# Optimization experiments

Hardware: AMD Instinct MI355X
Metric: run time of the kernel (lower is better)

Reference implementation:

```python
import jax, jax.numpy as jnp
import numpy as np

B, S, H, NH = 2, 2048, 1024, 16
HD = H // NH


def setup_inputs() -> dict:
    key = jax.random.key(0)
    ks = jax.random.split(key, 14)
    lim = 1.0 / np.sqrt(H)  # torch Linear default init range
    def lin(ka, kb):
        W = jax.random.uniform(ka, (H, H), jnp.float32, -lim, lim)
        b = jax.random.uniform(kb, (H,), jnp.float32, -lim, lim)
        return W, b
    Wq, bq = lin(ks[0], ks[1])
    Wk, bk = lin(ks[2], ks[3])
    Wv, bv = lin(ks[4], ks[5])
    Wo, bo = lin(ks[6], ks[7])
    return {
        "query": jax.random.normal(ks[8], (B, S, H), jnp.float32),
        "key": jax.random.normal(ks[9], (B, S, H), jnp.float32),
        "value": jax.random.normal(ks[10], (B, S, H), jnp.float32),
        "attn_mask": jax.random.randint(ks[11], (B, S, S), 0, 2).astype(bool),
        "relative_time": jax.random.normal(ks[12], (B, 1, S, S), jnp.float32),
        "Wq": Wq, "bq": bq, "Wk": Wk, "bk": bk,
        "Wv": Wv, "bv": bv, "Wo": Wo, "bo": bo,
    }


def reference(query, key, value, attn_mask, relative_time,
              Wq, bq, Wk, bk, Wv, bv, Wo, bo):
    Bq, Sq, _ = query.shape
    Skv = key.shape[1]
    # projections (torch Linear: x @ W^T + b)
    Q = (query @ Wq.T + bq).reshape(Bq, Sq, NH, HD).transpose(0, 2, 1, 3)
    K = (key @ Wk.T + bk).reshape(Bq, Skv, NH, HD).transpose(0, 2, 1, 3)
    V = (value @ Wv.T + bv).reshape(Bq, Skv, NH, HD).transpose(0, 2, 1, 3)
    scale = HD ** (-0.5)
    # NOTE: bias added BEFORE scaling, matching the original (non-standard)
    scores = jnp.einsum("bhqd,bhkd->bhqk", Q, K)
    scores = (scores + relative_time) * scale
    scores = jnp.where(attn_mask[:, None, :, :], scores, -jnp.inf)
    attn = jax.nn.softmax(scores.astype(jnp.float32), axis=-1).astype(scores.dtype)
    attn = jnp.nan_to_num(attn, nan=0.0)
    # dropout is identity in eval mode (dropout_rate applied only when training)
    out = jnp.einsum("bhqk,bhkd->bhqd", attn, V)
    out = out.transpose(0, 2, 1, 3).reshape(Bq, Sq, H)
    return out @ Wo.T + bo
```

## Files before the change

### kernel.cpp

```cpp
#include <hip/hip_runtime.h>
#include <hip/hip_bf16.h>

constexpr int BATCH = 2, SEQ = 2048, HDIM = 1024, NHEADS = 16, HEADD = 64;
constexpr int MROWS = BATCH * SEQ;
constexpr float QSCALE = 0.18033688011112042f;

typedef short short8  __attribute__((ext_vector_type(8)));
typedef float f32x4   __attribute__((ext_vector_type(4)));
typedef float f32x16  __attribute__((ext_vector_type(16)));
typedef int   int4v   __attribute__((ext_vector_type(4)));
typedef unsigned short ushort4v __attribute__((ext_vector_type(4)));

static __device__ __forceinline__ short f2bf(float f) {
    __hip_bfloat16 h = __float2bfloat16(f);
    return *reinterpret_cast<short*>(&h);
}

static __device__ __forceinline__ int cvt_pk_bf16(float a, float b) {
    int r;
    asm("v_cvt_pk_bf16_f32 %0, %1, %2" : "=v"(r) : "v"(a), "v"(b));
    return r;
}

static __device__ __forceinline__ float bfbits2f(unsigned short u) {
    return __builtin_bit_cast(float, (unsigned int)u << 16);
}

static __device__ __forceinline__ void gload_lds16(const void* g, void* l) {
    __builtin_amdgcn_global_load_lds(
        (const __attribute__((address_space(1))) unsigned int*)g,
        (__attribute__((address_space(3))) unsigned int*)l, 16, 0, 0);
}

__global__ void cvt_qkv_kernel(const float* __restrict__ q, const float* __restrict__ k,
                               const float* __restrict__ v, short* __restrict__ xq,
                               short* __restrict__ xk, short* __restrict__ xv, int n4) {
    int i = blockIdx.x * blockDim.x + threadIdx.x;
    const int stride = gridDim.x * blockDim.x;
    for (; i < 3 * n4; i += stride) {
        const float* in; short* out; int j = i;
        if (j >= 2 * n4)      { in = v; out = xv; j -= 2 * n4; }
        else if (j >= n4)     { in = k; out = xk; j -= n4; }
        else                  { in = q; out = xq; }
        const float4 val = reinterpret_cast<const float4*>(in)[j];
        short4 o;
        o.x = f2bf(val.x); o.y = f2bf(val.y); o.z = f2bf(val.z); o.w = f2bf(val.w);
        reinterpret_cast<short4*>(out)[j] = o;
    }
}

__global__ void cvt_w4_kernel(const float* __restrict__ w0, const float* __restrict__ w1,
                              const float* __restrict__ w2, const float* __restrict__ w3,
                              short* __restrict__ o0, short* __restrict__ o1,
                              short* __restrict__ o2, short* __restrict__ o3, int n4) {
    int i = blockIdx.x * blockDim.x + threadIdx.x;
    const int stride = gridDim.x * blockDim.x;
    for (; i < 4 * n4; i += stride) {
        const float* in; short* out; int j = i;
        if (j >= 3 * n4)      { in = w3; out = o3; j -= 3 * n4; }
        else if (j >= 2 * n4) { in = w2; out = o2; j -= 2 * n4; }
        else if (j >= n4)     { in = w1; out = o1; j -= n4; }
        else                  { in = w0; out = o0; }
        const float4 val = reinterpret_cast<const float4*>(in)[j];
        short4 o;
        o.x = f2bf(val.x); o.y = f2bf(val.y); o.z = f2bf(val.z); o.w = f2bf(val.w);
        reinterpret_cast<short4*>(out)[j] = o;
    }
}

__global__ void detect_mask_kernel(const unsigned int* __restrict__ m, int* flag) {
    const int tid = threadIdx.x;
    int gt1 = 0, isf = 0;
    for (int i = 0; i < 4; ++i) {
        unsigned int wv = m[tid + 256 * i];
        if (wv > 1u) gt1 = 1;
        if (wv == 0x3F800000u) isf = 1;
    }
    __shared__ int s_gt1, s_isf;
    if (tid == 0) { s_gt1 = 0; s_isf = 0; }
    __syncthreads();
    if (gt1) atomicOr(&s_gt1, 1);
    if (isf) atomicOr(&s_isf, 1);
    __syncthreads();
    if (tid == 0) flag[0] = s_gt1 ? (s_isf ? 2 : 1) : 0;
}

__global__ void fuse_rel_kernel(const float* __restrict__ rel, const void* __restrict__ mask,
                                const int* __restrict__ flag, short* __restrict__ rT,
                                int nThr) {
    const int f = flag[0];
    int i = blockIdx.x * blockDim.x + threadIdx.x;
    const int stride = gridDim.x * blockDim.x;
    for (; i < nThr; i += stride) {
        const int q    = i & 2047;
        const int kv16 = (i >> 11) & 127;
        const int b    = i >> 18;
        const long base = ((long)(b * 2048 + q)) * 2048 + kv16 * 16;
        float4 rv[4];
        #pragma unroll
        for (int g = 0; g < 4; ++g)
            rv[g] = *reinterpret_cast<const float4*>(rel + base + 4 * g);
        bool mk[16];
        if (f == 1) {
            const unsigned int* mp = (const unsigned int*)((const unsigned char*)mask + base);
            #pragma unroll
            for (int wd = 0; wd < 4; ++wd) {
                const unsigned int mw = mp[wd];
                #pragma unroll
                for (int s = 0; s < 4; ++s) mk[wd * 4 + s] = ((mw >> (8 * s)) & 0xffu) != 0;
            }
        } else if (f == 0) {
            const int* mp = (const int*)mask + base;
            #pragma unroll
            for (int j = 0; j < 16; ++j) mk[j] = mp[j] != 0;
        } else {
            const float* mp = (const float*)mask + base;
            #pragma unroll
            for (int j = 0; j < 16; ++j) mk[j] = mp[j] != 0.0f;
        }
        const float* rp = reinterpret_cast<const float*>(&rv[0]);
        #pragma unroll
        for (int g = 0; g < 4; ++g) {
            short4 o;
            short* op = reinterpret_cast<short*>(&o);
            #pragma unroll
            for (int j = 0; j < 4; ++j) {
                const int idx = 4 * g + j;
                op[j] = f2bf(mk[idx] ? rp[idx] * QSCALE : -1e30f);
            }
            *reinterpret_cast<short4*>(rT + (((long)(b * 512 + kv16 * 4 + g)) * 2048 + q) * 4) = o;
        }
    }
}

template<typename EPI>
static __device__ __forceinline__
void gemm_core(const short* A, const short* Bw, int K, int m0, int n0, EPI epi) {
    __shared__ short As[128 * 64];
    __shared__ short Bs[128 * 64];
    const int tid  = threadIdx.x;
    const int lane = tid & 63;
    const int w    = tid >> 6;
    const int lo   = lane & 15, hi = lane >> 4;
    const int wm   = w >> 1, wn = w & 1;

    f32x4 acc[4][4] = {};

    const int arow = tid >> 3;
    const int acol = (tid & 7) * 8;
    const long aBase = (long)(m0 + arow) * K + acol;
    const long bBase = (long)(n0 + arow) * K + acol;

    for (int k0 = 0; k0 < K; k0 += 64) {
        for (int i = 0; i < 4; ++i) {
            gload_lds16(A  + aBase + (long)i * 32 * K + k0, (char*)As + i * 4096 + tid * 16);
            gload_lds16(Bw + bBase + (long)i * 32 * K + k0, (char*)Bs + i * 4096 + tid * 16);
        }
        __syncthreads();
        for (int ks = 0; ks < 2; ++ks) {
            short8 af[4], bf[4];
            const int koff = ks * 32 + hi * 8;
            for (int fm = 0; fm < 4; ++fm)
                af[fm] = *reinterpret_cast<const short8*>(&As[(wm * 64 + fm * 16 + lo) * 64 + koff]);
            for (int fn = 0; fn < 4; ++fn)
                bf[fn] = *reinterpret_cast<const short8*>(&Bs[(wn * 64 + fn * 16 + lo) * 64 + koff]);
            for (int fm = 0; fm < 4; ++fm)
                for (int fn = 0; fn < 4; ++fn)
                    acc[fm][fn] = __builtin_amdgcn_mfma_f32_16x16x32_bf16(
                        af[fm], bf[fn], acc[fm][fn], 0, 0, 0);
        }
        __syncthreads();
    }

    for (int fm = 0; fm < 4; ++fm)
        for (int fn = 0; fn < 4; ++fn) {
            const int n = n0 + wn * 64 + fn * 16 + lo;
            const int mB = m0 + wm * 64 + fm * 16 + hi * 4;
            for (int r = 0; r < 4; ++r) epi(mB + r, n, acc[fm][fn][r]);
        }
}

__global__ __launch_bounds__(256, 2)
void qkv_gemm(const short* xq, const short* xk, const short* xv,
              const short* wq, const short* wk, const short* wv,
              const float* bq, const float* bk, const float* bv,
              short* Qb, short* Kb, short* Vt) {
    const int which = blockIdx.x >> 8;
    const int bid   = blockIdx.x & 255;
    const int m0 = (bid >> 3) << 7;
    const int n0 = (bid & 7) << 7;
    const short* A    = which == 0 ? xq : which == 1 ? xk : xv;
    const short* W    = which == 0 ? wq : which == 1 ? wk : wv;
    const float* bias = which == 0 ? bq : which == 1 ? bk : bv;
    short* C          = which == 0 ? Qb : which == 1 ? Kb : Vt;
    const float scale = which == 0 ? QSCALE : 1.0f;
    gemm_core(A, W, HDIM, m0, n0, [&](int m, int n, float v) {
        v = (v + bias[n]) * scale;
        const int b = m >> 11, s = m & (SEQ - 1);
        const int h = n >> 6, d = n & 63;
        long idx;
        if (which != 2) idx = (((long)(b * NHEADS + h)) * SEQ + s) * HEADD + d;
        else            idx = (((long)(b * NHEADS + h)) * HEADD + d) * SEQ + s;
        C[idx] = f2bf(v);
    });
}

__global__ __launch_bounds__(256, 2)
void out_gemm(const short* A, const short* W, const float* bias, float* Cout) {
    const int bid = blockIdx.x;
    const int m0 = (bid >> 3) << 7;
    const int n0 = (bid & 7) << 7;
    gemm_core(A, W, HDIM, m0, n0, [&](int m, int n, float v) {
        Cout[(long)m * HDIM + n] = v + bias[n];
    });
}

__global__ __launch_bounds__(256, 2)
void attn_fwd(const short* __restrict__ Qb, const short* __restrict__ Kb,
              const short* __restrict__ Vtb, const short* __restrict__ rT,
              short* __restrict__ Ob) {
    __shared__ short Ks[2][64 * 64];
    __shared__ short Vs[2][64 * 64];
    const int tid  = threadIdx.x;
    const int lane = tid & 63;
    const int wq   = tid >> 6;
    const int l31  = lane & 31, hi2 = lane >> 5;
    const int wg = ((blockIdx.x & 7) << 6) + (blockIdx.x >> 3);
    const int qt = wg & 15, h = (wg >> 4) & 15, b = wg >> 8;
    const int bh = b * NHEADS + h;
    const int q0 = qt * 128 + wq * 32 + l31;

    short8 qf[4];
    {
        const short* qp = Qb + ((long)bh * SEQ + q0) * HEADD + hi2 * 8;
        #pragma unroll
        for (int s = 0; s < 4; ++s)
            qf[s] = *reinterpret_cast<const short8*>(qp + s * 16);
    }

    float lsum = 0.0f;
    f32x16 oacc0 = {}, oacc1 = {};

    const int srow  = tid >> 3;
    const int scolb = (tid & 7) * 16;
    const int scolK = scolb ^ ((srow & 7) << 4);
    const char* KbB = (const char*)Kb + ((long)bh * SEQ + srow) * 128 + scolK;
    const char* VbB = (const char*)Vtb + ((long)bh * HEADD + srow) * ((long)SEQ * 2) + scolK;

    auto stage = [&](int buf, int kt) {
        #pragma unroll
        for (int i = 0; i < 2; ++i) {
            gload_lds16(KbB + ((long)kt * 64 + i * 32) * 128,
                        (char*)&Ks[buf][0] + i * 4096 + tid * 16);
            gload_lds16(VbB + (long)i * 32 * (SEQ * 2) + (long)kt * 128,
                        (char*)&Vs[buf][0] + i * 4096 + tid * 16);
        }
    };

    ushort4v rbuf[8];
    auto loadRel = [&](int kt) {
        #pragma unroll
        for (int t = 0; t < 2; ++t)
            #pragma unroll
            for (int g = 0; g < 4; ++g) {
                const int p4 = kt * 16 + t * 8 + 2 * g + hi2;
                rbuf[t * 4 + g] = *reinterpret_cast<const ushort4v*>(
                    rT + (((long)(b * 512 + p4)) * 2048 + q0) * 4);
            }
    };

    stage(0, 0);
    loadRel(0);
    __syncthreads();

    const int rsw = (l31 & 7) << 4;

    for (int kt = 0; kt < SEQ / 64; ++kt) {
        const int cb = kt & 1;
        if (kt < SEQ / 64 - 1) stage(cb ^ 1, kt + 1);

        f32x16 sc[2];
        #pragma unroll
        for (int t = 0; t < 2; ++t)
            #pragma unroll
            for (int g = 0; g < 4; ++g)
                #pragma unroll
                for (int j = 0; j < 4; ++j)
                    sc[t][4 * g + j] = bfbits2f(rbuf[t * 4 + g][j]);
        loadRel(kt < SEQ / 64 - 1 ? kt + 1 : 0);

        const char* kls = (const char*)&Ks[cb][0];
        __builtin_amdgcn_s_setprio(1);
        #pragma unroll
        for (int t = 0; t < 2; ++t) {
            const char* kr = kls + (t * 32 + l31) * 128;
            #pragma unroll
            for (int s = 0; s < 4; ++s) {
                short8 kf = *reinterpret_cast<const short8*>(kr + ((s * 32 + hi2 * 16) ^ rsw));
                sc[t] = __builtin_amdgcn_mfma_f32_32x32x16_bf16(kf, qf[s], sc[t], 0, 0, 0);
            }
        }
        __builtin_amdgcn_s_setprio(0);

        int pa[4][4];
        #pragma unroll
        for (int t = 0; t < 2; ++t) {
            int X[8];
            #pragma unroll
            for (int i2 = 0; i2 < 8; ++i2) {
                const float p0 = __builtin_amdgcn_exp2f(sc[t][2 * i2]);
                const float p1 = __builtin_amdgcn_exp2f(sc[t][2 * i2 + 1]);
                lsum += p0 + p1;
                X[i2] = cvt_pk_bf16(p0, p1);
            }
            #pragma unroll
            for (int u = 0; u < 2; ++u) {
                auto r0 = __builtin_amdgcn_permlane32_swap(X[4 * u + 0], X[4 * u + 2], false, false);
                auto r1 = __builtin_amdgcn_permlane32_swap(X[4 * u + 1], X[4 * u + 3], false, false);
                pa[2 * t + u][0] = (int)r0[0];
                pa[2 * t + u][1] = (int)r1[0];
                pa[2 * t + u][2] = (int)r0[1];
                pa[2 * t + u][3] = (int)r1[1];
            }
        }

        const char* vls = (const char*)&Vs[cb][0];
        __builtin_amdgcn_s_setprio(1);
        #pragma unroll
        for (int dt = 0; dt < 2; ++dt) {
            const char* vr = vls + (dt * 32 + l31) * 128;
            #pragma unroll
            for (int s = 0; s < 4; ++s) {
                short8 vf = *reinterpret_cast<const short8*>(vr + ((s * 32 + hi2 * 16) ^ rsw));
                int4v pw = { pa[s][0], pa[s][1], pa[s][2], pa[s][3] };
                if (dt == 0)
                    oacc0 = __builtin_amdgcn_mfma_f32_32x32x16_bf16(
                        __builtin_bit_cast(short8, pw), vf, oacc0, 0, 0, 0);
                else
                    oacc1 = __builtin_amdgcn_mfma_f32_32x32x16_bf16(
                        __builtin_bit_cast(short8, pw), vf, oacc1, 0, 0, 0);
            }
        }
        __builtin_amdgcn_s_setprio(0);
        __syncthreads();
    }

    lsum += __shfl_xor(lsum, 32, 64);
    const float inv = lsum > 0.0f ? 1.0f / lsum : 0.0f;

    #pragma unroll
    for (int r = 0; r < 16; ++r) {
        const int qloc = (r & 3) + 8 * (r >> 2) + 4 * hi2;
        const float invr = __shfl(inv, qloc, 64);
        const int qg = qt * 128 + wq * 32 + qloc;
        const long obase = ((long)b * SEQ + qg) * HDIM + h * 64 + l31;
        Ob[obase]      = f2bf(oacc0[r] * invr);
        Ob[obase + 32] = f2bf(oacc1[r] * invr);
    }
}

extern "C" void kernel_launch(void* const* d_in, const int* in_sizes, int n_in,
                              void* d_out, int out_size, void* d_ws, size_t ws_size,
                              hipStream_t stream) {
    const float* q    = (const float*)d_in[0];
    const float* k    = (const float*)d_in[1];
    const float* v    = (const float*)d_in[2];
    const void*  mask = d_in[3];
    const float* rel  = (const float*)d_in[4];
    const float* Wq   = (const float*)d_in[5];
    const float* bq   = (const float*)d_in[6];
    const float* Wk   = (const float*)d_in[7];
    const float* bk   = (const float*)d_in[8];
    const float* Wv   = (const float*)d_in[9];
    const float* bv   = (const float*)d_in[10];
    const float* Wo   = (const float*)d_in[11];
    const float* bo   = (const float*)d_in[12];
    (void)in_sizes; (void)n_in; (void)out_size; (void)ws_size;

    char* ws = (char*)d_ws;
    size_t off = 0;
    auto alloc = [&](size_t bytes) {
        char* p = ws + off;
        off += (bytes + 255) & ~(size_t)255;
        return p;
    };
    const size_t xBytes = (size_t)MROWS * HDIM * 2;
    const size_t wBytes = (size_t)HDIM * HDIM * 2;
    const size_t poolBytes = 3 * xBytes + 3 * wBytes;

    short* Qb  = (short*)alloc(xBytes);
    short* Kb  = (short*)alloc(xBytes);
    short* Vt  = (short*)alloc(xBytes);
    short* wob = (short*)alloc(wBytes);
    int*   flag = (int*)alloc(256);
    char* pool = (char*)alloc(poolBytes);
    short* Ab  = (short*)alloc(xBytes);

    short* xq  = (short*)(pool);
    short* xk  = (short*)(pool + xBytes);
    short* xv  = (short*)(pool + 2 * xBytes);
    short* wqb = (short*)(pool + 3 * xBytes);
    short* wkb = (short*)(pool + 3 * xBytes + wBytes);
    short* wvb = (short*)(pool + 3 * xBytes + 2 * wBytes);
    short* rT  = (short*)(pool);

    const int n4x = MROWS * HDIM / 4, n4w = HDIM * HDIM / 4;
    cvt_qkv_kernel<<<1024, 256, 0, stream>>>(q, k, v, xq, xk, xv, n4x);
    cvt_w4_kernel<<<512, 256, 0, stream>>>(Wq, Wk, Wv, Wo, wqb, wkb, wvb, wob, n4w);
    detect_mask_kernel<<<1, 256, 0, stream>>>((const unsigned int*)mask, flag);

    qkv_gemm<<<768, 256, 0, stream>>>(xq, xk, xv, wqb, wkb, wvb,
                                      bq, bk, bv, Qb, Kb, Vt);

    const int relThr = BATCH * 128 * 2048;
    fuse_rel_kernel<<<2048, 256, 0, stream>>>(rel, mask, flag, rT, relThr);

    attn_fwd<<<512, 256, 0, stream>>>(Qb, Kb, Vt, rT, Ab);

    out_gemm<<<256, 256, 0, stream>>>(Ab, wob, bo, (float*)d_out);
}
```

Measured before the change: 168.9 us.

## Split attention key tiles across wave pairs and merge the two conversion kernels

The attention kernel now covers 64 query rows per block instead of 128. Its four waves form two query halves times two key halves, and each wave handles 32 of the 64 keys in every tile. Partial outputs and row sums are combined through shared memory at the end. The grid doubles to 1024 blocks, and launch bounds rise to 4 blocks per SM to raise occupancy and cut per-wave register pressure. The cost is that K/V tiles are loaded once per 64 queries instead of once per 128, doubling K/V traffic, and a reduction plus barrier is added at the end. Separately, the input and weight fp32-to-bf16 conversion kernels are fused into a single launch.

```diff
diff --git a/kernel.cpp b/kernel.cpp
--- a/kernel.cpp
+++ b/kernel.cpp
@@ -32,35 +32,30 @@
         (__attribute__((address_space(3))) unsigned int*)l, 16, 0, 0);
 }
 
-__global__ void cvt_qkv_kernel(const float* __restrict__ q, const float* __restrict__ k,
-                               const float* __restrict__ v, short* __restrict__ xq,
-                               short* __restrict__ xk, short* __restrict__ xv, int n4) {
+__global__ void cvt_all_kernel(const float* __restrict__ q, const float* __restrict__ k,
+                               const float* __restrict__ v, const float* __restrict__ w0,
+                               const float* __restrict__ w1, const float* __restrict__ w2,
+                               const float* __restrict__ w3,
+                               short* __restrict__ xq, short* __restrict__ xk,
+                               short* __restrict__ xv, short* __restrict__ o0,
+                               short* __restrict__ o1, short* __restrict__ o2,
+                               short* __restrict__ o3, int n4x, int n4w) {
     int i = blockIdx.x * blockDim.x + threadIdx.x;
     const int stride = gridDim.x * blockDim.x;
-    for (; i < 3 * n4; i += stride) {
+    const int total = 3 * n4x + 4 * n4w;
+    for (; i < total; i += stride) {
         const float* in; short* out; int j = i;
-        if (j >= 2 * n4)      { in = v; out = xv; j -= 2 * n4; }
-        else if (j >= n4)     { in = k; out = xk; j -= n4; }
-        else                  { in = q; out = xq; }
-        const float4 val = reinterpret_cast<const float4*>(in)[j];
-        short4 o;
-        o.x = f2bf(val.x); o.y = f2bf(val.y); o.z = f2bf(val.z); o.w = f2bf(val.w);
-        reinterpret_cast<short4*>(out)[j] = o;
-    }
-}
-
-__global__ void cvt_w4_kernel(const float* __restrict__ w0, const float* __restrict__ w1,
-                              const float* __restrict__ w2, const float* __restrict__ w3,
-                              short* __restrict__ o0, short* __restrict__ o1,
-                              short* __restrict__ o2, short* __restrict__ o3, int n4) {
-    int i = blockIdx.x * blockDim.x + threadIdx.x;
-    const int stride = gridDim.x * blockDim.x;
-    for (; i < 4 * n4; i += stride) {
-        const float* in; short* out; int j = i;
-        if (j >= 3 * n4)      { in = w3; out = o3; j -= 3 * n4; }
-        else if (j >= 2 * n4) { in = w2; out = o2; j -= 2 * n4; }
-        else if (j >= n4)     { in = w1; out = o1; j -= n4; }
-        else                  { in = w0; out = o0; }
+        if (j < 3 * n4x) {
+            if (j >= 2 * n4x)      { in = v; out = xv; j -= 2 * n4x; }
+            else if (j >= n4x)     { in = k; out = xk; j -= n4x; }
+            else                   { in = q; out = xq; }
+        } else {
+            j -= 3 * n4x;
+            if (j >= 3 * n4w)      { in = w3; out = o3; j -= 3 * n4w; }
+            else if (j >= 2 * n4w) { in = w2; out = o2; j -= 2 * n4w; }
+            else if (j >= n4w)     { in = w1; out = o1; j -= n4w; }
+            else                   { in = w0; out = o0; }
+        }
         const float4 val = reinterpret_cast<const float4*>(in)[j];
         short4 o;
         o.x = f2bf(val.x); o.y = f2bf(val.y); o.z = f2bf(val.z); o.w = f2bf(val.w);
@@ -215,7 +210,7 @@
     });
 }
 
-__global__ __launch_bounds__(256, 2)
+__global__ __launch_bounds__(256, 4)
 void attn_fwd(const short* __restrict__ Qb, const short* __restrict__ Kb,
               const short* __restrict__ Vtb, const short* __restrict__ rT,
               short* __restrict__ Ob) {
@@ -223,19 +218,21 @@
     __shared__ short Vs[2][64 * 64];
     const int tid  = threadIdx.x;
     const int lane = tid & 63;
-    const int wq   = tid >> 6;
+    const int wv   = tid >> 6;
+    const int qp   = wv & 1;
+    const int t    = wv >> 1;
     const int l31  = lane & 31, hi2 = lane >> 5;
-    const int wg = ((blockIdx.x & 7) << 6) + (blockIdx.x >> 3);
-    const int qt = wg & 15, h = (wg >> 4) & 15, b = wg >> 8;
+    const int wg = ((blockIdx.x & 7) << 7) + (blockIdx.x >> 3);
+    const int qt = wg & 31, h = (wg >> 5) & 15, b = wg >> 9;
     const int bh = b * NHEADS + h;
-    const int q0 = qt * 128 + wq * 32 + l31;
+    const int q0 = qt * 64 + qp * 32 + l31;
 
     short8 qf[4];
     {
-        const short* qp = Qb + ((long)bh * SEQ + q0) * HEADD + hi2 * 8;
+        const short* qp_ = Qb + ((long)bh * SEQ + q0) * HEADD + hi2 * 8;
         #pragma unroll
         for (int s = 0; s < 4; ++s)
-            qf[s] = *reinterpret_cast<const short8*>(qp + s * 16);
+            qf[s] = *reinterpret_cast<const short8*>(qp_ + s * 16);
     }
 
     float lsum = 0.0f;
@@ -257,16 +254,14 @@
         }
     };
 
-    ushort4v rbuf[8];
+    ushort4v rbuf[4];
     auto loadRel = [&](int kt) {
         #pragma unroll
-        for (int t = 0; t < 2; ++t)
-            #pragma unroll
-            for (int g = 0; g < 4; ++g) {
-                const int p4 = kt * 16 + t * 8 + 2 * g + hi2;
-                rbuf[t * 4 + g] = *reinterpret_cast<const ushort4v*>(
-                    rT + (((long)(b * 512 + p4)) * 2048 + q0) * 4);
-            }
+        for (int g = 0; g < 4; ++g) {
+            const int p4 = kt * 16 + t * 8 + 2 * g + hi2;
+            rbuf[g] = *reinterpret_cast<const ushort4v*>(
+                rT + (((long)(b * 512 + p4)) * 2048 + q0) * 4);
+        }
     };
 
     stage(0, 0);
@@ -279,49 +274,41 @@
         const int cb = kt & 1;
         if (kt < SEQ / 64 - 1) stage(cb ^ 1, kt + 1);
 
-        f32x16 sc[2];
-        #pragma unroll
-        for (int t = 0; t < 2; ++t)
-            #pragma unroll
-            for (int g = 0; g < 4; ++g)
-                #pragma unroll
-                for (int j = 0; j < 4; ++j)
-                    sc[t][4 * g + j] = bfbits2f(rbuf[t * 4 + g][j]);
+        f32x16 sc;
+        #pragma unroll
+        for (int g = 0; g < 4; ++g)
+            #pragma unroll
+            for (int j = 0; j < 4; ++j)
+                sc[4 * g + j] = bfbits2f(rbuf[g][j]);
         loadRel(kt < SEQ / 64 - 1 ? kt + 1 : 0);
 
         const char* kls = (const char*)&Ks[cb][0];
+        const char* kr  = kls + (t * 32 + l31) * 128;
         __builtin_amdgcn_s_setprio(1);
         #pragma unroll
-        for (int t = 0; t < 2; ++t) {
-            const char* kr = kls + (t * 32 + l31) * 128;
-            #pragma unroll
-            for (int s = 0; s < 4; ++s) {
-                short8 kf = *reinterpret_cast<const short8*>(kr + ((s * 32 + hi2 * 16) ^ rsw));
-                sc[t] = __builtin_amdgcn_mfma_f32_32x32x16_bf16(kf, qf[s], sc[t], 0, 0, 0);
-            }
+        for (int s = 0; s < 4; ++s) {
+            short8 kf = *reinterpret_cast<const short8*>(kr + ((s * 32 + hi2 * 16) ^ rsw));
+            sc = __builtin_amdgcn_mfma_f32_32x32x16_bf16(kf, qf[s], sc, 0, 0, 0);
         }
         __builtin_amdgcn_s_setprio(0);
 
-        int pa[4][4];
-        #pragma unroll
-        for (int t = 0; t < 2; ++t) {
-            int X[8];
-            #pragma unroll
-            for (int i2 = 0; i2 < 8; ++i2) {
-                const float p0 = __builtin_amdgcn_exp2f(sc[t][2 * i2]);
-                const float p1 = __builtin_amdgcn_exp2f(sc[t][2 * i2 + 1]);
-                lsum += p0 + p1;
-                X[i2] = cvt_pk_bf16(p0, p1);
-            }
-            #pragma unroll
-            for (int u = 0; u < 2; ++u) {
-                auto r0 = __builtin_amdgcn_permlane32_swap(X[4 * u + 0], X[4 * u + 2], false, false);
-                auto r1 = __builtin_amdgcn_permlane32_swap(X[4 * u + 1], X[4 * u + 3], false, false);
-                pa[2 * t + u][0] = (int)r0[0];
-                pa[2 * t + u][1] = (int)r1[0];
-                pa[2 * t + u][2] = (int)r0[1];
-                pa[2 * t + u][3] = (int)r1[1];
-            }
+        int X[8];
+        #pragma unroll
+        for (int i2 = 0; i2 < 8; ++i2) {
+            const float p0 = __builtin_amdgcn_exp2f(sc[2 * i2]);
+            const float p1 = __builtin_amdgcn_exp2f(sc[2 * i2 + 1]);
+            lsum += p0 + p1;
+            X[i2] = cvt_pk_bf16(p0, p1);
+        }
+        int pa[2][4];
+        #pragma unroll
+        for (int u = 0; u < 2; ++u) {
+            auto r0 = __builtin_amdgcn_permlane32_swap(X[4 * u + 0], X[4 * u + 2], false, false);
+            auto r1 = __builtin_amdgcn_permlane32_swap(X[4 * u + 1], X[4 * u + 3], false, false);
+            pa[u][0] = (int)r0[0];
+            pa[u][1] = (int)r1[0];
+            pa[u][2] = (int)r0[1];
+            pa[u][3] = (int)r1[1];
         }
 
         const char* vls = (const char*)&Vs[cb][0];
@@ -330,9 +317,10 @@
         for (int dt = 0; dt < 2; ++dt) {
             const char* vr = vls + (dt * 32 + l31) * 128;
             #pragma unroll
-            for (int s = 0; s < 4; ++s) {
+            for (int u = 0; u < 2; ++u) {
+                const int s = 2 * t + u;
                 short8 vf = *reinterpret_cast<const short8*>(vr + ((s * 32 + hi2 * 16) ^ rsw));
-                int4v pw = { pa[s][0], pa[s][1], pa[s][2], pa[s][3] };
+                int4v pw = { pa[u][0], pa[u][1], pa[u][2], pa[u][3] };
                 if (dt == 0)
                     oacc0 = __builtin_amdgcn_mfma_f32_32x32x16_bf16(
                         __builtin_bit_cast(short8, pw), vf, oacc0, 0, 0, 0);
@@ -346,16 +334,33 @@
     }
 
     lsum += __shfl_xor(lsum, 32, 64);
-    const float inv = lsum > 0.0f ? 1.0f / lsum : 0.0f;
-
-    #pragma unroll
-    for (int r = 0; r < 16; ++r) {
-        const int qloc = (r & 3) + 8 * (r >> 2) + 4 * hi2;
-        const float invr = __shfl(inv, qloc, 64);
-        const int qg = qt * 128 + wq * 32 + qloc;
-        const long obase = ((long)b * SEQ + qg) * HDIM + h * 64 + l31;
-        Ob[obase]      = f2bf(oacc0[r] * invr);
-        Ob[obase + 32] = f2bf(oacc1[r] * invr);
+
+    float* cmbO = (float*)&Ks[0][0];
+    float* cmbL = (float*)&Vs[0][0];
+    if (t == 1) {
+        #pragma unroll
+        for (int r = 0; r < 16; ++r) {
+            const int qloc = (r & 3) + 8 * (r >> 2) + 4 * hi2;
+            cmbO[(qp * 32 + qloc) * 64 + l31]      = oacc0[r];
+            cmbO[(qp * 32 + qloc) * 64 + 32 + l31] = oacc1[r];
+        }
+        if (hi2 == 0) cmbL[qp * 32 + l31] = lsum;
+    }
+    __syncthreads();
+    if (t == 0) {
+        const float ltot = lsum + cmbL[qp * 32 + l31];
+        const float inv  = ltot > 0.0f ? 1.0f / ltot : 0.0f;
+        #pragma unroll
+        for (int r = 0; r < 16; ++r) {
+            const int qloc = (r & 3) + 8 * (r >> 2) + 4 * hi2;
+            const float invr = __shfl(inv, qloc, 64);
+            const int qg = qt * 64 + qp * 32 + qloc;
+            const long obase = ((long)b * SEQ + qg) * HDIM + h * 64 + l31;
+            const float o0 = oacc0[r] + cmbO[(qp * 32 + qloc) * 64 + l31];
+            const float o1 = oacc1[r] + cmbO[(qp * 32 + qloc) * 64 + 32 + l31];
+            Ob[obase]      = f2bf(o0 * invr);
+            Ob[obase + 32] = f2bf(o1 * invr);
+        }
     }
 }
 
@@ -405,8 +410,8 @@
     short* rT  = (short*)(pool);
 
     const int n4x = MROWS * HDIM / 4, n4w = HDIM * HDIM / 4;
-    cvt_qkv_kernel<<<1024, 256, 0, stream>>>(q, k, v, xq, xk, xv, n4x);
-    cvt_w4_kernel<<<512, 256, 0, stream>>>(Wq, Wk, Wv, Wo, wqb, wkb, wvb, wob, n4w);
+    cvt_all_kernel<<<2048, 256, 0, stream>>>(q, k, v, Wq, Wk, Wv, Wo,
+                                             xq, xk, xv, wqb, wkb, wvb, wob, n4x, n4w);
     detect_mask_kernel<<<1, 256, 0, stream>>>((const unsigned int*)mask, flag);
 
     qkv_gemm<<<768, 256, 0, stream>>>(xq, xk, xv, wqb, wkb, wvb,
@@ -415,7 +420,7 @@
     const int relThr = BATCH * 128 * 2048;
     fuse_rel_kernel<<<2048, 256, 0, stream>>>(rel, mask, flag, rT, relThr);
 
-    attn_fwd<<<512, 256, 0, stream>>>(Qb, Kb, Vt, rT, Ab);
+    attn_fwd<<<1024, 256, 0, stream>>>(Qb, Kb, Vt, rT, Ab);
 
     out_gemm<<<256, 256, 0, stream>>>(Ab, wob, bo, (float*)d_out);
 }
```

Measured after the change: 169.3 us. About the same (+0.2%).
